# Kernel optimization log

Measured on AMD Instinct MI355X. Metric: run time of the kernel, lower is better.

Reference implementation:

```python
import jax, jax.numpy as jnp
import numpy as np
from jax import lax

B, L, E = 2, 2048, 1024          # batch, seq_len, embed_dim
NL = 2                            # n_layers
DI = 2 * E                        # d_inner (expand=2)
DS = 16                           # d_state
DC = 4                            # d_conv
DTR = (E + 15) // 16              # dt_rank = ceil(d_model/16) = 64


def setup_inputs() -> dict:
    key = jax.random.key(0)
    ks = jax.random.split(key, 12)
    s = 0.02
    inp = {
        "x": jax.random.normal(ks[0], (B, L, E), jnp.float32),
        "pos_embed": jax.random.normal(ks[1], (L, E), jnp.float32) * s,
        "in_proj_w": jax.random.normal(ks[2], (NL, 2 * DI, E), jnp.float32) * s,
        "conv_w": jax.random.normal(ks[3], (NL, DI, DC), jnp.float32) * s,
        "conv_b": jnp.zeros((NL, DI), jnp.float32),
        "x_proj_w": jax.random.normal(ks[4], (NL, DTR + 2 * DS, DI), jnp.float32) * s,
        "dt_proj_w": jax.random.normal(ks[5], (NL, DI, DTR), jnp.float32) * s,
        "dt_bias": jax.random.normal(ks[6], (NL, DI), jnp.float32) * 0.1,
        "A_log": jnp.broadcast_to(jnp.log(jnp.arange(1, DS + 1, dtype=jnp.float32)), (NL, DI, DS)) + 0.0,
        "D_skip": jnp.ones((NL, DI), jnp.float32),
        "out_proj_w": jax.random.normal(ks[7], (NL, E, DI), jnp.float32) * s,
        "norm_w": jnp.ones((NL, E), jnp.float32),
    }
    return inp


def _rmsnorm(x, w, eps=1e-6):
    return x * lax.rsqrt(jnp.mean(x * x, axis=-1, keepdims=True) + eps) * w


def _mamba(h, in_w, cw, cb, xw, dtw, dtb, A_log, Dp, ow):
    # h: (B, L, E)
    xz = jnp.einsum("ble,de->bld", h, in_w)          # (B, L, 2*DI)
    xc, z = jnp.split(xz, 2, axis=-1)                 # each (B, L, DI)
    # causal depthwise conv1d (kernel DC)
    xp = jnp.pad(xc, ((0, 0), (DC - 1, 0), (0, 0)))
    xconv = cb
    acc = jnp.zeros_like(xc)
    for k in range(DC):
        acc = acc + cw[:, k] * xp[:, k:k + xc.shape[1], :]
    xc = jax.nn.silu(acc + cb)
    # input-dependent SSM params
    x_dbl = jnp.einsum("bld,rd->blr", xc, xw)         # (B, L, DTR+2*DS)
    dt, Bm, C = jnp.split(x_dbl, [DTR, DTR + DS], axis=-1)
    delta = jax.nn.softplus(jnp.einsum("blr,dr->bld", dt, dtw) + dtb)  # (B, L, DI)
    A = -jnp.exp(A_log)                               # (DI, DS)

    def step(hst, inp):
        d, bm, c, u = inp                             # (B,DI),(B,DS),(B,DS),(B,DI)
        hst = jnp.exp(d[..., None] * A) * hst + (d * u)[..., None] * bm[:, None, :]
        y = jnp.einsum("bdn,bn->bd", hst, c)
        return hst, y

    h0 = jnp.zeros((h.shape[0], DI, DS), h.dtype)
    _, ys = lax.scan(step, h0, (delta.swapaxes(0, 1), Bm.swapaxes(0, 1),
                                C.swapaxes(0, 1), xc.swapaxes(0, 1)))
    y = ys.swapaxes(0, 1) + xc * Dp                   # (B, L, DI)
    y = y * jax.nn.silu(z)
    return jnp.einsum("bld,ed->ble", y, ow)


def reference(x, pos_embed, in_proj_w, conv_w, conv_b, x_proj_w, dt_proj_w,
              dt_bias, A_log, D_skip, out_proj_w, norm_w):
    h = x + pos_embed[None, :x.shape[1]]
    for i in range(in_proj_w.shape[0]):
        y = _mamba(h, in_proj_w[i], conv_w[i], conv_b[i], x_proj_w[i],
                   dt_proj_w[i], dt_bias[i], A_log[i], D_skip[i], out_proj_w[i])
        h = _rmsnorm(y + h, norm_w[i])
    return h
```

## Files before the change

### kernel.cpp

```cpp
#include <hip/hip_runtime.h>

#define B_   2
#define L_   2048
#define E_   1024
#define NL_  2
#define DI_  2048
#define DS_  16
#define DC_  4
#define DTR_ 64
#define NXD_ 96
#define M_   (B_ * L_)
#define NCH_ 64
#define LC_  32

typedef __attribute__((ext_vector_type(8))) short bf16x8;
typedef __attribute__((ext_vector_type(4))) float f32x4;

__device__ __forceinline__ float bf2f(unsigned short u) {
    return __uint_as_float(((unsigned)u) << 16);
}
__device__ __forceinline__ unsigned short f2bf(float f) {
    unsigned u = __float_as_uint(f);
    u += 0x7fff + ((u >> 16) & 1);
    return (unsigned short)(u >> 16);
}

#define LOG2E_ 1.44269504f
#define LN2_   0.69314718f

__device__ __forceinline__ float sigmoidf_(float x) {
    return __builtin_amdgcn_rcpf(1.f + __builtin_amdgcn_exp2f(-x * LOG2E_));
}
__device__ __forceinline__ float softplusf_(float x) {
    float e = __builtin_amdgcn_exp2f(x * LOG2E_);
    float s = LN2_ * __builtin_amdgcn_logf(1.f + e);
    return x > 15.f ? x : s;
}
__device__ __forceinline__ float expf_(float x) {
    return __builtin_amdgcn_exp2f(x * LOG2E_);
}
__device__ __forceinline__ float ldin(const void* p, size_t i, int isbf) {
    return isbf ? bf2f(((const unsigned short*)p)[i]) : ((const float*)p)[i];
}
__device__ __forceinline__ void gld_lds16(const unsigned short* g, unsigned short* l) {
    __builtin_amdgcn_global_load_lds(
        (const __attribute__((address_space(1))) unsigned int*)g,
        (__attribute__((address_space(3))) unsigned int*)l, 16, 0, 0);
}

__device__ __forceinline__ void expvec(int fast, float dv, const float* a2, float* e) {
    if (fast) {
        float p1 = __builtin_amdgcn_exp2f(dv * a2[0]);
        float p2 = p1 * p1, p4 = p2 * p2, p8 = p4 * p4;
        e[0] = p1;        e[1] = p2;        e[2] = p2 * p1;   e[3] = p4;
        e[4] = p4 * p1;   e[5] = p4 * p2;   e[6] = e[5] * p1; e[7] = p8;
        e[8] = p8 * p1;   e[9] = p8 * p2;   e[10] = e[9] * p1; e[11] = p8 * p4;
        e[12] = e[11] * p1; e[13] = e[11] * p2; e[14] = e[13] * p1; e[15] = p8 * p8;
    } else {
#pragma unroll
        for (int n = 0; n < 16; ++n) e[n] = __builtin_amdgcn_exp2f(dv * a2[n]);
    }
}

__global__ __launch_bounds__(256) void detect_kernel(const unsigned* __restrict__ x,
                                                     int* __restrict__ flags)
{
    __shared__ int cnt;
    if (threadIdx.x == 0) cnt = 0;
    __syncthreads();
    unsigned v = x[threadIdx.x];
    int e = (v >> 7) & 0xFF;
    if (e >= 90 && e <= 140) atomicAdd(&cnt, 1);
    __syncthreads();
    if (threadIdx.x == 0) {
        flags[0] = (cnt >= 192) ? 1 : 0;
        flags[1] = 1;
        flags[2] = 1;
    }
}

__global__ __launch_bounds__(256) void chk_alog(
    const void* __restrict__ alog, int* __restrict__ flags)
{
    int isbf = flags[0];
    int i = blockIdx.x * 256 + threadIdx.x;
    int layer = i / (DI_ * DS_);
    int n = i & (DS_ - 1);
    float a  = -expf_(ldin(alog, i, isbf));
    float a0 = -expf_(ldin(alog, i - n, isbf));
    float want = (n + 1) * a0;
    if (fabsf(a - want) > 0.02f * fabsf(want))
        atomicAnd(&flags[1 + layer], 0);
}

#define WB_IN_  0
#define WB_XW_  4194304
#define WB_DTW_ 4456448
#define WB_OW_  4587520
#define WB_TOT_ 6684672
__global__ __launch_bounds__(256) void cvt_layer_kernel(
    const void* __restrict__ inw, const void* __restrict__ xw,
    const void* __restrict__ dtw, const void* __restrict__ ow,
    int layer, unsigned short* __restrict__ wbuf, const int* __restrict__ flag)
{
    int isbf = *flag;
    int i = blockIdx.x * 256 + threadIdx.x;
    unsigned short v;
    if (i < WB_XW_) {
        v = isbf ? ((const unsigned short*)inw)[(size_t)layer * 2 * DI_ * E_ + i]
                 : f2bf(((const float*)inw)[(size_t)layer * 2 * DI_ * E_ + i]);
    } else if (i < WB_DTW_) {
        int j = i - WB_XW_; int r = j >> 11, k = j & (DI_ - 1);
        v = (r < NXD_)
          ? (isbf ? ((const unsigned short*)xw)[(size_t)layer * NXD_ * DI_ + (size_t)r * DI_ + k]
                  : f2bf(((const float*)xw)[(size_t)layer * NXD_ * DI_ + (size_t)r * DI_ + k]))
          : (unsigned short)0;
    } else if (i < WB_OW_) {
        int j = i - WB_DTW_;
        v = isbf ? ((const unsigned short*)dtw)[(size_t)layer * DI_ * DTR_ + j]
                 : f2bf(((const float*)dtw)[(size_t)layer * DI_ * DTR_ + j]);
    } else {
        int j = i - WB_OW_;
        v = isbf ? ((const unsigned short*)ow)[(size_t)layer * E_ * DI_ + j]
                 : f2bf(((const float*)ow)[(size_t)layer * E_ * DI_ + j]);
    }
    wbuf[i] = v;
}

__global__ __launch_bounds__(256) void add_pos_kernel(
    const void* __restrict__ x, const void* __restrict__ pos,
    float* __restrict__ h, unsigned short* __restrict__ h16,
    const int* __restrict__ flag)
{
    int isbf = *flag;
    int i = blockIdx.x * 256 + threadIdx.x;
    float v = ldin(x, i, isbf) + ldin(pos, i & (L_ * E_ - 1), isbf);
    h[i] = v;
    h16[i] = f2bf(v);
}

__global__ __launch_bounds__(256) void gemm_mfma(
    const unsigned short* __restrict__ A, int lda,
    const unsigned short* __restrict__ W, int ldw,
    void* __restrict__ C, int ldc, int Ksplit, size_t cSliceStride,
    const void* __restrict__ bias, size_t boff,
    void* __restrict__ C2, int ep, const int* __restrict__ flag)
{
    __shared__ unsigned short As[128 * 64];
    __shared__ unsigned short Bs[128 * 64];
    int tid = threadIdx.x;
    int lane = tid & 63, w = tid >> 6;
    int m0 = blockIdx.x * 128, n0 = blockIdx.y * 128;
    int wm = (w >> 1) * 64, wn = (w & 1) * 64;
    int col = lane & 15, quad = lane >> 4;
    int kstart = blockIdx.z * Ksplit;

    f32x4 acc[4][4];
#pragma unroll
    for (int i = 0; i < 4; ++i)
#pragma unroll
        for (int j = 0; j < 4; ++j)
            acc[i][j] = (f32x4){0.f, 0.f, 0.f, 0.f};

    for (int kt = kstart; kt < kstart + Ksplit; kt += 64) {
#pragma unroll
        for (int i = 0; i < 4; ++i) {
            int seg = i * 4 + w;
            int q = seg * 64 + lane;
            int r = q >> 3, cd = q & 7;
            int cs = cd ^ (r & 7);
            gld_lds16(A + (size_t)(m0 + r) * lda + kt + cs * 8, &As[seg * 512]);
            gld_lds16(W + (size_t)(n0 + r) * ldw + kt + cs * 8, &Bs[seg * 512]);
        }
        __syncthreads();
#pragma unroll
        for (int ks = 0; ks < 2; ++ks) {
            bf16x8 af[4], bfr[4];
#pragma unroll
            for (int t = 0; t < 4; ++t) {
                int rowA = wm + t * 16 + col;
                int ca = ks * 4 + quad;
                af[t]  = *(const bf16x8*)&As[rowA * 64 + ((ca ^ (rowA & 7)) * 8)];
                int rowB = wn + t * 16 + col;
                bfr[t] = *(const bf16x8*)&Bs[rowB * 64 + ((ca ^ (rowB & 7)) * 8)];
            }
#pragma unroll
            for (int tm = 0; tm < 4; ++tm)
#pragma unroll
                for (int tn = 0; tn < 4; ++tn)
                    acc[tm][tn] = __builtin_amdgcn_mfma_f32_16x16x32_bf16(
                        af[tm], bfr[tn], acc[tm][tn], 0, 0, 0);
        }
        __syncthreads();
    }

    int isbf = flag ? *flag : 1;
    if (ep == 4) {
        unsigned short* dst = (n0 < DI_) ? (unsigned short*)C : (unsigned short*)C2;
        int nsub = (n0 < DI_) ? n0 : n0 - DI_;
#pragma unroll
        for (int tm = 0; tm < 4; ++tm)
#pragma unroll
            for (int tn = 0; tn < 4; ++tn)
#pragma unroll
                for (int rg = 0; rg < 4; ++rg) {
                    int gm = m0 + wm + tm * 16 + quad * 4 + rg;
                    int gn = nsub + wn + tn * 16 + col;
                    dst[(size_t)gm * DI_ + gn] = f2bf(acc[tm][tn][rg]);
                }
        return;
    }
    float* Cp = (float*)C + (size_t)blockIdx.z * cSliceStride;
#pragma unroll
    for (int tm = 0; tm < 4; ++tm)
#pragma unroll
        for (int tn = 0; tn < 4; ++tn)
#pragma unroll
            for (int rg = 0; rg < 4; ++rg) {
                int gm = m0 + wm + tm * 16 + quad * 4 + rg;
                int gn = n0 + wn + tn * 16 + col;
                float v = acc[tm][tn][rg];
                if (ep == 0) {
                    Cp[(size_t)gm * ldc + gn] = v;
                } else {
                    v = softplusf_(v + ldin(bias, boff + gn, isbf));
                    ((unsigned short*)C)[(size_t)gm * ldc + gn] = f2bf(v);
                }
            }
}

#define G8_NT (E_ / 32)
__global__ __launch_bounds__(512) void gemm_inproj8(
    const unsigned short* __restrict__ A,
    const unsigned short* __restrict__ W,
    unsigned short* __restrict__ Cx,
    unsigned short* __restrict__ Cz)
{
    __shared__ unsigned short lds[65536];
    int tid = threadIdx.x;
    int lane = tid & 63, w = tid >> 6;
    int wr = w >> 2, wc = w & 3;
    int col = lane & 15, quad = lane >> 4;

    int flat = blockIdx.y * 16 + blockIdx.x;
    int nn = (flat & 7) * 32 + (flat >> 3);
    int cch = nn >> 5, wi = nn & 31;
    int bx = (cch & 3) * 4 + (wi & 3);
    int by = (cch >> 2) * 8 + (wi >> 2);
    int m0 = bx * 256, n0 = by * 256;

    const unsigned short* srcA = A + (size_t)(m0 + (lane & 15)) * E_ + (lane >> 4) * 8;
    const unsigned short* srcW = W + (size_t)(n0 + (lane & 15)) * E_ + (lane >> 4) * 8;

    f32x4 acc[8][4];
#pragma unroll
    for (int i = 0; i < 8; ++i)
#pragma unroll
        for (int j = 0; j < 4; ++j)
            acc[i][j] = (f32x4){0.f, 0.f, 0.f, 0.f};

#pragma unroll
    for (int tp = 0; tp < 3; ++tp) {
#pragma unroll
        for (int s = 0; s < 2; ++s) {
            int seg = s * 8 + w;
            gld_lds16(srcA + (size_t)seg * 16 * E_ + tp * 32, &lds[tp * 16384 + seg * 512]);
            gld_lds16(srcW + (size_t)seg * 16 * E_ + tp * 32, &lds[tp * 16384 + 8192 + seg * 512]);
        }
    }

    for (int t = 0; t < G8_NT; ++t) {
        if (t < G8_NT - 2)       asm volatile("s_waitcnt vmcnt(8)" ::: "memory");
        else if (t == G8_NT - 2) asm volatile("s_waitcnt vmcnt(4)" ::: "memory");
        else                     asm volatile("s_waitcnt vmcnt(0)" ::: "memory");
        __builtin_amdgcn_s_barrier();

        int cb = (t & 3) * 16384;
        int sb = ((t + 3) & 3) * 16384;
        int kt = (t + 3) * 32;
        bool dost = (t + 3) < G8_NT;

        bf16x8 bfr[4];
#pragma unroll
        for (int tn = 0; tn < 4; ++tn)
            bfr[tn] = *(const bf16x8*)&lds[cb + 8192 + (wc * 4 + tn) * 512 + quad * 128 + col * 8];

#pragma unroll
        for (int mh = 0; mh < 2; ++mh) {
            bf16x8 af[4];
#pragma unroll
            for (int t4 = 0; t4 < 4; ++t4)
                af[t4] = *(const bf16x8*)&lds[cb + (wr * 8 + mh * 4 + t4) * 512 + quad * 128 + col * 8];
            if (dost) {
                int seg = mh * 8 + w;
                gld_lds16(srcA + (size_t)seg * 16 * E_ + kt, &lds[sb + seg * 512]);
                gld_lds16(srcW + (size_t)seg * 16 * E_ + kt, &lds[sb + 8192 + seg * 512]);
            }
            __builtin_amdgcn_s_barrier();
            __builtin_amdgcn_s_setprio(1);
#pragma unroll
            for (int t4 = 0; t4 < 4; ++t4)
#pragma unroll
                for (int tn = 0; tn < 4; ++tn)
                    acc[mh * 4 + t4][tn] = __builtin_amdgcn_mfma_f32_16x16x32_bf16(
                        af[t4], bfr[tn], acc[mh * 4 + t4][tn], 0, 0, 0);
            __builtin_amdgcn_s_setprio(0);
            __builtin_amdgcn_s_barrier();
        }
    }

    unsigned short* dst = (n0 < DI_) ? Cx : Cz;
    int nb = (n0 < DI_) ? n0 : n0 - DI_;
#pragma unroll
    for (int tm = 0; tm < 8; ++tm)
#pragma unroll
        for (int tn = 0; tn < 4; ++tn)
#pragma unroll
            for (int rg = 0; rg < 4; ++rg) {
                int gm = m0 + wr * 128 + tm * 16 + quad * 4 + rg;
                int gn = nb + wc * 64 + tn * 16 + col;
                dst[(size_t)gm * DI_ + gn] = f2bf(acc[tm][tn][rg]);
            }
}

__global__ __launch_bounds__(256) void xproj_reduce(
    const float* __restrict__ part, float* __restrict__ xdbl,
    unsigned short* __restrict__ dt16)
{
    int i = blockIdx.x * 256 + threadIdx.x;
    int r = i >> 7, c = i & 127;
    float v = 0.f;
#pragma unroll
    for (int s = 0; s < 8; ++s) v += part[(size_t)s * (M_ * 128) + i];
    if (c < NXD_) xdbl[(size_t)r * NXD_ + c] = v;
    if (c < DTR_) dt16[(size_t)r * DTR_ + c] = f2bf(v);
}

__global__ __launch_bounds__(256) void conv_silu_kernel(
    const unsigned short* __restrict__ xcr16, const void* __restrict__ cw, size_t cwoff,
    const void* __restrict__ cb, size_t cboff, unsigned short* __restrict__ xc16,
    const int* __restrict__ flag)
{
    int isbf = *flag;
    int i = blockIdx.x * 256 + threadIdx.x;
    int d = i & (DI_ - 1);
    int bl = i >> 11;
    int l = bl & (L_ - 1);
    float acc = ldin(cb, cboff + d, isbf);
#pragma unroll
    for (int k = 0; k < DC_; ++k) {
        int ls = l - (DC_ - 1) + k;
        if (ls >= 0)
            acc += ldin(cw, cwoff + d * DC_ + k, isbf)
                 * bf2f(xcr16[(size_t)(bl - (DC_ - 1) + k) * DI_ + d]);
    }
    xc16[i] = f2bf(acc * sigmoidf_(acc));
}

__global__ __launch_bounds__(256) void scan_part1(
    const unsigned short* __restrict__ dl16, const unsigned short* __restrict__ xc16,
    const float* __restrict__ xdbl,
    const void* __restrict__ A_log, size_t aoff,
    float* __restrict__ sumdbuf, float* __restrict__ scrS,
    const int* __restrict__ flags, int layer)
{
    int isbf = flags[0], fast = flags[1 + layer];
    __shared__ float bs[LC_][16];
    int c = blockIdx.y;
    int b = blockIdx.x >> 3;
    int d = ((blockIdx.x & 7) << 8) + threadIdx.x;
    for (int i = threadIdx.x; i < LC_ * 16; i += 256) {
        int l = i >> 4, n = i & 15;
        bs[l][n] = xdbl[((size_t)b * L_ + c * LC_ + l) * NXD_ + DTR_ + n];
    }
    __syncthreads();
    float a2[16];
#pragma unroll
    for (int n = 0; n < 16; ++n)
        a2[n] = -expf_(ldin(A_log, aoff + (size_t)d * DS_ + n, isbf)) * LOG2E_;
    float s[16] = {};
    float sumd = 0.f;
    const unsigned short* dp = dl16 + ((size_t)b * L_ + c * LC_) * DI_ + d;
    const unsigned short* up = xc16 + ((size_t)b * L_ + c * LC_) * DI_ + d;
    for (int l = 0; l < LC_; ++l) {
        float dv = bf2f(dp[(size_t)l * DI_]);
        float u  = bf2f(up[(size_t)l * DI_]);
        sumd += dv;
        float dvu = dv * u;
        float e[16];
        expvec(fast, dv, a2, e);
        float4 b0 = *(const float4*)&bs[l][0];
        float4 b1 = *(const float4*)&bs[l][4];
        float4 b2 = *(const float4*)&bs[l][8];
        float4 b3 = *(const float4*)&bs[l][12];
        float bv[16] = {b0.x,b0.y,b0.z,b0.w, b1.x,b1.y,b1.z,b1.w,
                        b2.x,b2.y,b2.z,b2.w, b3.x,b3.y,b3.z,b3.w};
#pragma unroll
        for (int n = 0; n < 16; ++n)
            s[n] = fmaf(e[n], s[n], dvu * bv[n]);
    }
    int g = b * DI_ + d;
    sumdbuf[(size_t)c * (B_ * DI_) + g] = sumd;
    size_t base = ((size_t)c * (B_ * DI_) + g) * 16;
#pragma unroll
    for (int q = 0; q < 4; ++q)
        *(float4*)&scrS[base + q * 4] =
            make_float4(s[q*4], s[q*4+1], s[q*4+2], s[q*4+3]);
}

__global__ __launch_bounds__(256) void scan_combine(
    const float* __restrict__ sumdbuf, float* __restrict__ scrS,
    const void* __restrict__ A_log, size_t aoff, const int* __restrict__ flags)
{
    int isbf = flags[0];
    int t = blockIdx.x * 256 + threadIdx.x;
    int g = t >> 4, n = t & 15;
    int d = g & (DI_ - 1);
    float a2 = -expf_(ldin(A_log, aoff + (size_t)d * DS_ + n, isbf)) * LOG2E_;
    float sd[NCH_], sl[NCH_];
#pragma unroll
    for (int c = 0; c < NCH_; ++c) {
        sd[c] = sumdbuf[(size_t)c * (B_ * DI_) + g];
        sl[c] = scrS[(size_t)c * (B_ * DI_ * 16) + t];
    }
    float s = 0.f;
#pragma unroll
    for (int c = 0; c < NCH_; ++c) {
        float P = __builtin_amdgcn_exp2f(a2 * sd[c]);
        float nxt = fmaf(P, s, sl[c]);
        scrS[(size_t)c * (B_ * DI_ * 16) + t] = s;
        s = nxt;
    }
}

__global__ __launch_bounds__(256) void scan_part2(
    const unsigned short* __restrict__ dl16, unsigned short* __restrict__ xc16,
    const float* __restrict__ xdbl, const unsigned short* __restrict__ z,
    const void* __restrict__ A_log, size_t aoff,
    const void* __restrict__ Dskip, size_t doff,
    const float* __restrict__ scrS, const int* __restrict__ flags, int layer)
{
    int isbf = flags[0], fast = flags[1 + layer];
    __shared__ float bs[LC_][32];
    int c = blockIdx.y;
    int b = blockIdx.x >> 3;
    int d = ((blockIdx.x & 7) << 8) + threadIdx.x;
    for (int i = threadIdx.x; i < LC_ * 32; i += 256) {
        int l = i >> 5, n = i & 31;
        bs[l][n] = xdbl[((size_t)b * L_ + c * LC_ + l) * NXD_ + DTR_ + n];
    }
    __syncthreads();
    float a2[16];
#pragma unroll
    for (int n = 0; n < 16; ++n)
        a2[n] = -expf_(ldin(A_log, aoff + (size_t)d * DS_ + n, isbf)) * LOG2E_;
    float Dv = ldin(Dskip, doff + d, isbf);
    int g = b * DI_ + d;
    size_t sbase = ((size_t)c * (B_ * DI_) + g) * 16;
    float s[16];
#pragma unroll
    for (int q = 0; q < 4; ++q) {
        float4 sv = *(const float4*)&scrS[sbase + q * 4];
        s[q*4] = sv.x; s[q*4+1] = sv.y; s[q*4+2] = sv.z; s[q*4+3] = sv.w;
    }

    const unsigned short* dp = dl16 + ((size_t)b * L_ + c * LC_) * DI_ + d;
    unsigned short* up = xc16 + ((size_t)b * L_ + c * LC_) * DI_ + d;
    const unsigned short* zp = z + ((size_t)b * L_ + c * LC_) * DI_ + d;
    for (int l = 0; l < LC_; ++l) {
        float dv = bf2f(dp[(size_t)l * DI_]);
        float u  = bf2f(up[(size_t)l * DI_]);
        float dvu = dv * u;
        float e[16];
        expvec(fast, dv, a2, e);
        float4 b0 = *(const float4*)&bs[l][0];
        float4 b1 = *(const float4*)&bs[l][4];
        float4 b2 = *(const float4*)&bs[l][8];
        float4 b3 = *(const float4*)&bs[l][12];
        float4 c0 = *(const float4*)&bs[l][16];
        float4 c1 = *(const float4*)&bs[l][20];
        float4 c2 = *(const float4*)&bs[l][24];
        float4 c3 = *(const float4*)&bs[l][28];
        float bv[16] = {b0.x,b0.y,b0.z,b0.w, b1.x,b1.y,b1.z,b1.w,
                        b2.x,b2.y,b2.z,b2.w, b3.x,b3.y,b3.z,b3.w};
        float cv[16] = {c0.x,c0.y,c0.z,c0.w, c1.x,c1.y,c1.z,c1.w,
                        c2.x,c2.y,c2.z,c2.w, c3.x,c3.y,c3.z,c3.w};
        float y = 0.f;
#pragma unroll
        for (int n = 0; n < 16; ++n) {
            s[n] = fmaf(e[n], s[n], dvu * bv[n]);
            y = fmaf(s[n], cv[n], y);
        }
        float zv = bf2f(zp[(size_t)l * DI_]);
        up[(size_t)l * DI_] = f2bf((y + u * Dv) * (zv * sigmoidf_(zv)));
    }
}

__global__ __launch_bounds__(256) void rmsnorm_kernel(
    const float* __restrict__ y0, const float* __restrict__ y1,
    float* __restrict__ h, unsigned short* __restrict__ h16,
    const void* __restrict__ nw, size_t nwoff, void* __restrict__ out,
    int write_out, const int* __restrict__ flag)
{
    int isbf = *flag;
    __shared__ float red[4];
    int row = blockIdx.x;
    float* hp = h + (size_t)row * E_;
    float v[4]; float ss = 0.f;
#pragma unroll
    for (int i = 0; i < 4; ++i) {
        int e = threadIdx.x + i * 256;
        size_t idx = (size_t)row * E_ + e;
        v[i] = y0[idx] + y1[idx] + hp[e];
        ss += v[i] * v[i];
    }
#pragma unroll
    for (int off = 1; off < 64; off <<= 1) ss += __shfl_xor(ss, off, 64);
    if ((threadIdx.x & 63) == 0) red[threadIdx.x >> 6] = ss;
    __syncthreads();
    ss = red[0] + red[1] + red[2] + red[3];
    float scale = rsqrtf(ss * (1.f / E_) + 1e-6f);
#pragma unroll
    for (int i = 0; i < 4; ++i) {
        int e = threadIdx.x + i * 256;
        float hv = v[i] * scale * ldin(nw, nwoff + e, isbf);
        hp[e] = hv;
        h16[(size_t)row * E_ + e] = f2bf(hv);
        if (write_out) {
            size_t oi = (size_t)row * E_ + e;
            if (isbf) ((unsigned short*)out)[oi] = f2bf(hv);
            else      ((float*)out)[oi] = hv;
        }
    }
}

extern "C" void kernel_launch(void* const* d_in, const int* in_sizes, int n_in,
                              void* d_out, int out_size, void* d_ws, size_t ws_size,
                              hipStream_t stream)
{
    const void* x    = d_in[0];
    const void* pos  = d_in[1];
    const void* inw  = d_in[2];
    const void* cw   = d_in[3];
    const void* cb   = d_in[4];
    const void* xw   = d_in[5];
    const void* dtw  = d_in[6];
    const void* dtb  = d_in[7];
    const void* alog = d_in[8];
    const void* dsk  = d_in[9];
    const void* ow   = d_in[10];
    const void* nw   = d_in[11];

    float* ws = (float*)d_ws;
    float* h      = ws;
    unsigned short* h16  = (unsigned short*)(ws + 4194304);
    unsigned short* z16  = (unsigned short*)(ws + 6291456);
    unsigned short* xc16 = (unsigned short*)(ws + 10485760);
    float* D      = ws + 14680064;
    float* R      = ws + 23068672;
    float* xdbl   = ws + 27262976;
    unsigned short* dt16 = (unsigned short*)(ws + 27656192);
    float* sumd   = ws + 27787264;
    unsigned short* wbuf = (unsigned short*)(ws + 28049408);
    int* flags    = (int*)(ws + 31391744);

    unsigned short* xcr16 = (unsigned short*)R;
    float* xp_part = R;
    float* scrS    = R;
    unsigned short* dl16 = (unsigned short*)D;
    float* yout0 = D;
    float* yout1 = D + (size_t)M_ * E_;

    detect_kernel<<<1, 256, 0, stream>>>((const unsigned*)x, flags);
    chk_alog<<<NL_ * DI_ * DS_ / 256, 256, 0, stream>>>(alog, flags);
    add_pos_kernel<<<M_ * E_ / 256, 256, 0, stream>>>(x, pos, h, h16, flags);

    for (int layer = 0; layer < NL_; ++layer) {
        cvt_layer_kernel<<<WB_TOT_ / 256, 256, 0, stream>>>(
            inw, xw, dtw, ow, layer, wbuf, flags);

        gemm_inproj8<<<dim3(M_ / 256, 2 * DI_ / 256, 1), 512, 0, stream>>>(
            h16, wbuf + WB_IN_, xcr16, z16);
        conv_silu_kernel<<<M_ * DI_ / 256, 256, 0, stream>>>(
            xcr16, cw, (size_t)layer * DI_ * DC_, cb, (size_t)layer * DI_, xc16, flags);
        gemm_mfma<<<dim3(M_ / 128, 1, 8), 256, 0, stream>>>(
            xc16, DI_, wbuf + WB_XW_, DI_, xp_part, 128, DI_ / 8, (size_t)M_ * 128,
            nullptr, 0, nullptr, 0, flags);
        xproj_reduce<<<M_ * 128 / 256, 256, 0, stream>>>(xp_part, xdbl, dt16);
        gemm_mfma<<<dim3(M_ / 128, DI_ / 128, 1), 256, 0, stream>>>(
            dt16, DTR_, wbuf + WB_DTW_, DTR_, dl16, DI_, DTR_, 0,
            dtb, (size_t)layer * DI_, nullptr, 2, flags);
        scan_part1<<<dim3(B_ * DI_ / 256, NCH_), 256, 0, stream>>>(
            dl16, xc16, xdbl, alog, (size_t)layer * DI_ * DS_, sumd, scrS, flags, layer);
        scan_combine<<<B_ * DI_ * DS_ / 256, 256, 0, stream>>>(
            sumd, scrS, alog, (size_t)layer * DI_ * DS_, flags);
        scan_part2<<<dim3(B_ * DI_ / 256, NCH_), 256, 0, stream>>>(
            dl16, xc16, xdbl, z16, alog, (size_t)layer * DI_ * DS_,
            dsk, (size_t)layer * DI_, scrS, flags, layer);
        gemm_mfma<<<dim3(M_ / 128, E_ / 128, 2), 256, 0, stream>>>(
            xc16, DI_, wbuf + WB_OW_, DI_, yout0, E_, DI_ / 2, (size_t)M_ * E_,
            nullptr, 0, nullptr, 0, flags);
        rmsnorm_kernel<<<M_, 256, 0, stream>>>(
            yout0, yout1, h, h16, nw, (size_t)layer * E_, d_out,
            layer == NL_ - 1 ? 1 : 0, flags);
    }
}
```

Baseline: 626.8 us.

## Vectorize causal conv with register sliding window; simplify in-proj GEMM pipeline

The per-element conv+SiLU kernel becomes a vectorized one. Each thread handles 8 channels across 4 timesteps, reads bf16x8 rows once and reuses them in a register sliding window, and takes conv weights pre-transposed to fp32 by a new small prep kernel. The in-proj GEMM main loop drops its split M-halves with mid-iteration barriers and issues all async loads up front, then runs all 32 MFMAs in one block. A dead ep==4 epilogue in gemm_mfma is also removed. The GEMM change may lose some load/compute interleaving, and it relies on the remaining loop-top barrier being enough to keep the LDS buffers safe.

```diff
diff --git a/kernel.cpp b/kernel.cpp
--- a/kernel.cpp
+++ b/kernel.cpp
@@ -195,21 +195,6 @@
     }
 
     int isbf = flag ? *flag : 1;
-    if (ep == 4) {
-        unsigned short* dst = (n0 < DI_) ? (unsigned short*)C : (unsigned short*)C2;
-        int nsub = (n0 < DI_) ? n0 : n0 - DI_;
-#pragma unroll
-        for (int tm = 0; tm < 4; ++tm)
-#pragma unroll
-            for (int tn = 0; tn < 4; ++tn)
-#pragma unroll
-                for (int rg = 0; rg < 4; ++rg) {
-                    int gm = m0 + wm + tm * 16 + quad * 4 + rg;
-                    int gn = nsub + wn + tn * 16 + col;
-                    dst[(size_t)gm * DI_ + gn] = f2bf(acc[tm][tn][rg]);
-                }
-        return;
-    }
     float* Cp = (float*)C + (size_t)blockIdx.z * cSliceStride;
 #pragma unroll
     for (int tm = 0; tm < 4; ++tm)
@@ -278,35 +263,32 @@
         int cb = (t & 3) * 16384;
         int sb = ((t + 3) & 3) * 16384;
         int kt = (t + 3) * 32;
-        bool dost = (t + 3) < G8_NT;
-
-        bf16x8 bfr[4];
-#pragma unroll
-        for (int tn = 0; tn < 4; ++tn)
-            bfr[tn] = *(const bf16x8*)&lds[cb + 8192 + (wc * 4 + tn) * 512 + quad * 128 + col * 8];
-
-#pragma unroll
-        for (int mh = 0; mh < 2; ++mh) {
-            bf16x8 af[4];
-#pragma unroll
-            for (int t4 = 0; t4 < 4; ++t4)
-                af[t4] = *(const bf16x8*)&lds[cb + (wr * 8 + mh * 4 + t4) * 512 + quad * 128 + col * 8];
-            if (dost) {
-                int seg = mh * 8 + w;
+
+        if ((t + 3) < G8_NT) {
+#pragma unroll
+            for (int s = 0; s < 2; ++s) {
+                int seg = s * 8 + w;
                 gld_lds16(srcA + (size_t)seg * 16 * E_ + kt, &lds[sb + seg * 512]);
                 gld_lds16(srcW + (size_t)seg * 16 * E_ + kt, &lds[sb + 8192 + seg * 512]);
             }
-            __builtin_amdgcn_s_barrier();
-            __builtin_amdgcn_s_setprio(1);
-#pragma unroll
-            for (int t4 = 0; t4 < 4; ++t4)
-#pragma unroll
-                for (int tn = 0; tn < 4; ++tn)
-                    acc[mh * 4 + t4][tn] = __builtin_amdgcn_mfma_f32_16x16x32_bf16(
-                        af[t4], bfr[tn], acc[mh * 4 + t4][tn], 0, 0, 0);
-            __builtin_amdgcn_s_setprio(0);
-            __builtin_amdgcn_s_barrier();
-        }
+        }
+
+        bf16x8 bfr[4], af[8];
+#pragma unroll
+        for (int tn = 0; tn < 4; ++tn)
+            bfr[tn] = *(const bf16x8*)&lds[cb + 8192 + (wc * 4 + tn) * 512 + quad * 128 + col * 8];
+#pragma unroll
+        for (int t8 = 0; t8 < 8; ++t8)
+            af[t8] = *(const bf16x8*)&lds[cb + (wr * 8 + t8) * 512 + quad * 128 + col * 8];
+
+        __builtin_amdgcn_s_setprio(1);
+#pragma unroll
+        for (int tm = 0; tm < 8; ++tm)
+#pragma unroll
+            for (int tn = 0; tn < 4; ++tn)
+                acc[tm][tn] = __builtin_amdgcn_mfma_f32_16x16x32_bf16(
+                    af[tm], bfr[tn], acc[tm][tn], 0, 0, 0);
+        __builtin_amdgcn_s_setprio(0);
     }
 
     unsigned short* dst = (n0 < DI_) ? Cx : Cz;
@@ -336,25 +318,70 @@
     if (c < DTR_) dt16[(size_t)r * DTR_ + c] = f2bf(v);
 }
 
-__global__ __launch_bounds__(256) void conv_silu_kernel(
-    const unsigned short* __restrict__ xcr16, const void* __restrict__ cw, size_t cwoff,
-    const void* __restrict__ cb, size_t cboff, unsigned short* __restrict__ xc16,
+__global__ __launch_bounds__(256) void conv_prep(
+    const void* __restrict__ cw, size_t cwoff, const void* __restrict__ cb,
+    size_t cboff, float* __restrict__ cwT, float* __restrict__ cbF,
     const int* __restrict__ flag)
 {
     int isbf = *flag;
-    int i = blockIdx.x * 256 + threadIdx.x;
-    int d = i & (DI_ - 1);
-    int bl = i >> 11;
-    int l = bl & (L_ - 1);
-    float acc = ldin(cb, cboff + d, isbf);
+    int d = blockIdx.x * 256 + threadIdx.x;
+#pragma unroll
+    for (int k = 0; k < DC_; ++k)
+        cwT[k * DI_ + d] = ldin(cw, cwoff + (size_t)d * DC_ + k, isbf);
+    cbF[d] = ldin(cb, cboff + d, isbf);
+}
+
+#define CT_ 4
+__global__ __launch_bounds__(256) void conv_silu_v(
+    const unsigned short* __restrict__ xcr16, const float* __restrict__ cwT,
+    const float* __restrict__ cbF, unsigned short* __restrict__ xc16)
+{
+    int g = blockIdx.x;
+    int bl0 = g * CT_;
+    int l0 = bl0 & (L_ - 1);
+    int d = threadIdx.x * 8;
+
+    float w[DC_][8], bias[8];
 #pragma unroll
     for (int k = 0; k < DC_; ++k) {
-        int ls = l - (DC_ - 1) + k;
-        if (ls >= 0)
-            acc += ldin(cw, cwoff + d * DC_ + k, isbf)
-                 * bf2f(xcr16[(size_t)(bl - (DC_ - 1) + k) * DI_ + d]);
-    }
-    xc16[i] = f2bf(acc * sigmoidf_(acc));
+        *(float4*)&w[k][0] = *(const float4*)&cwT[k * DI_ + d];
+        *(float4*)&w[k][4] = *(const float4*)&cwT[k * DI_ + d + 4];
+    }
+    *(float4*)&bias[0] = *(const float4*)&cbF[d];
+    *(float4*)&bias[4] = *(const float4*)&cbF[d + 4];
+
+    float xr[DC_ - 1 + CT_][8];
+#pragma unroll
+    for (int r = 0; r < DC_ - 1 + CT_; ++r) {
+        int l = l0 - (DC_ - 1) + r;
+        if (l >= 0) {
+            bf16x8 v = *(const bf16x8*)&xcr16[(size_t)(bl0 - (DC_ - 1) + r) * DI_ + d];
+#pragma unroll
+            for (int j = 0; j < 8; ++j) xr[r][j] = bf2f((unsigned short)v[j]);
+        } else {
+#pragma unroll
+            for (int j = 0; j < 8; ++j) xr[r][j] = 0.f;
+        }
+    }
+
+#pragma unroll
+    for (int t = 0; t < CT_; ++t) {
+        float acc[8];
+#pragma unroll
+        for (int j = 0; j < 8; ++j) acc[j] = bias[j];
+#pragma unroll
+        for (int k = 0; k < DC_; ++k)
+#pragma unroll
+            for (int j = 0; j < 8; ++j)
+                acc[j] = fmaf(w[k][j], xr[t + k][j], acc[j]);
+        bf16x8 ov;
+#pragma unroll
+        for (int j = 0; j < 8; ++j) {
+            float s = acc[j] * sigmoidf_(acc[j]);
+            ov[j] = (short)f2bf(s);
+        }
+        *(bf16x8*)&xc16[(size_t)(bl0 + t) * DI_ + d] = ov;
+    }
 }
 
 __global__ __launch_bounds__(256) void scan_part1(
@@ -570,6 +597,8 @@
     unsigned short* dl16 = (unsigned short*)D;
     float* yout0 = D;
     float* yout1 = D + (size_t)M_ * E_;
+    float* cwT = sumd;
+    float* cbF = sumd + DC_ * DI_;
 
     detect_kernel<<<1, 256, 0, stream>>>((const unsigned*)x, flags);
     chk_alog<<<NL_ * DI_ * DS_ / 256, 256, 0, stream>>>(alog, flags);
@@ -578,11 +607,12 @@
     for (int layer = 0; layer < NL_; ++layer) {
         cvt_layer_kernel<<<WB_TOT_ / 256, 256, 0, stream>>>(
             inw, xw, dtw, ow, layer, wbuf, flags);
+        conv_prep<<<DI_ / 256, 256, 0, stream>>>(
+            cw, (size_t)layer * DI_ * DC_, cb, (size_t)layer * DI_, cwT, cbF, flags);
 
         gemm_inproj8<<<dim3(M_ / 256, 2 * DI_ / 256, 1), 512, 0, stream>>>(
             h16, wbuf + WB_IN_, xcr16, z16);
-        conv_silu_kernel<<<M_ * DI_ / 256, 256, 0, stream>>>(
-            xcr16, cw, (size_t)layer * DI_ * DC_, cb, (size_t)layer * DI_, xc16, flags);
+        conv_silu_v<<<M_ / CT_, 256, 0, stream>>>(xcr16, cwT, cbF, xc16);
         gemm_mfma<<<dim3(M_ / 128, 1, 8), 256, 0, stream>>>(
             xc16, DI_, wbuf + WB_XW_, DI_, xp_part, 128, DI_ / 8, (size_t)M_ * 128,
             nullptr, 0, nullptr, 0, flags);
```

New measurement: 567.6 us. -9.4%, faster.
